# Optimization experiments

Measured on AMD Instinct MI355X. Metric: run time of the kernel, lower is better.

Reference implementation:

```python
import jax, jax.numpy as jnp
import numpy as np

E = 1024
FF = 4096
B, S = 4, 2048
EPS = 1e-5

def _layernorm(x, g, b):
    m = jnp.mean(x, axis=-1, keepdims=True)
    v = jnp.var(x, axis=-1, keepdims=True)
    return (x - m) * jax.lax.rsqrt(v + EPS) * g + b

def setup_inputs() -> dict:
    key = jax.random.key(0)
    ks = jax.random.split(key, 16)
    def lin(k, fan_in, shape):
        bound = 1.0 / np.sqrt(fan_in)
        return jax.random.uniform(k, shape, jnp.float32, -bound, bound)
    return {
        "src_embs": jax.random.normal(ks[0], (B, S, E), jnp.float32),
        "Wq_w": lin(ks[1], E, (E, E)), "Wq_b": lin(ks[2], E, (E,)),
        "Wk_w": lin(ks[3], E, (E, E)), "Wk_b": lin(ks[4], E, (E,)),
        "Wv_w": lin(ks[5], E, (E, E)), "Wv_b": lin(ks[6], E, (E,)),
        "Wo_w": lin(ks[7], E, (E, E)), "Wo_b": lin(ks[8], E, (E,)),
        "W1_w": lin(ks[9], E, (FF, E)), "W1_b": lin(ks[10], E, (FF,)),
        "W2_w": lin(ks[11], FF, (E, FF)), "W2_b": lin(ks[12], FF, (E,)),
        "g1": jnp.ones((E,), jnp.float32), "b1": jnp.zeros((E,), jnp.float32),
        "g2": jnp.ones((E,), jnp.float32), "b2": jnp.zeros((E,), jnp.float32),
        "g3": jnp.ones((E,), jnp.float32), "b3": jnp.zeros((E,), jnp.float32),
    }

def reference(src_embs, Wq_w, Wq_b, Wk_w, Wk_b, Wv_w, Wv_b, Wo_w, Wo_b,
              W1_w, W1_b, W2_w, W2_b, g1, b1, g2, b2, g3, b3):
    x = _layernorm(src_embs, g1, b1)
    Q = x @ Wq_w.T + Wq_b
    K = x @ Wk_w.T + Wk_b
    V = x @ Wv_w.T + Wv_b
    # single-head attention, scaled by sqrt(embed_dim) per source
    scores = jnp.einsum('bqe,bke->bqk', Q, K) / jnp.sqrt(jnp.float32(E))
    attn = jax.nn.softmax(scores, axis=-1)
    attn_out = jnp.einsum('bqk,bke->bqe', attn, V) @ Wo_w.T + Wo_b
    h = src_embs + attn_out
    hn = _layernorm(h, g2, b2)
    ff = jax.nn.relu(hn @ W1_w.T + W1_b) @ W2_w.T + W2_b
    out = h + ff
    return _layernorm(out, g3, b3)
```

## Files before the change

### kernel.cpp

```cpp
#include <hip/hip_runtime.h>
#include <cstdint>
#include <cmath>

#define E_DIM 1024
#define FF_DIM 4096
#define B_DIM 4
#define S_DIM 2048
#define NTOK (B_DIM * S_DIM)
#define QKV_N 3072

typedef __bf16 bf16;
typedef __attribute__((ext_vector_type(8))) __bf16 bf16x8;
typedef __attribute__((ext_vector_type(4))) float f32x4;

__device__ __forceinline__ void gload_lds16(const void* g, void* l) {
  __builtin_amdgcn_global_load_lds(
      (const __attribute__((address_space(1))) unsigned int*)g,
      (__attribute__((address_space(3))) unsigned int*)l, 16, 0, 0);
}

__device__ __forceinline__ float waveRedSum(float v) {
#pragma unroll
  for (int o = 32; o > 0; o >>= 1) v += __shfl_xor(v, o, 64);
  return v;
}
__device__ __forceinline__ float waveRedMax(float v) {
#pragma unroll
  for (int o = 32; o > 0; o >>= 1) v = fmaxf(v, __shfl_xor(v, o, 64));
  return v;
}

__global__ __launch_bounds__(256) void cvt_k(const float* __restrict__ in,
                                             bf16* __restrict__ out, int n4) {
  int i = blockIdx.x * 256 + threadIdx.x;
  if (i < n4) {
    float4 v = reinterpret_cast<const float4*>(in)[i];
    bf16* o = out + (size_t)i * 4;
    o[0] = (bf16)v.x; o[1] = (bf16)v.y; o[2] = (bf16)v.z; o[3] = (bf16)v.w;
  }
}

template <typename OutT>
__global__ __launch_bounds__(256) void layernorm_k(const float* __restrict__ x,
                                                   OutT* __restrict__ out,
                                                   const float* __restrict__ g,
                                                   const float* __restrict__ b) {
  const int row = blockIdx.x;
  const int tid = threadIdx.x;
  const float4 v = reinterpret_cast<const float4*>(x + (size_t)row * E_DIM)[tid];
  float s = v.x + v.y + v.z + v.w;
  float q = v.x * v.x + v.y * v.y + v.z * v.z + v.w * v.w;
  s = waveRedSum(s);
  q = waveRedSum(q);
  __shared__ float sa[4], sb[4];
  const int lane = tid & 63, wid = tid >> 6;
  if (lane == 0) { sa[wid] = s; sb[wid] = q; }
  __syncthreads();
  s = sa[0] + sa[1] + sa[2] + sa[3];
  q = sb[0] + sb[1] + sb[2] + sb[3];
  const float mean = s * (1.0f / E_DIM);
  const float var = q * (1.0f / E_DIM) - mean * mean;
  const float rstd = rsqrtf(var + 1e-5f);
  const int c = tid * 4;
  OutT* op = out + (size_t)row * E_DIM + c;
  const float vv[4] = {v.x, v.y, v.z, v.w};
#pragma unroll
  for (int j = 0; j < 4; ++j)
    op[j] = (OutT)((vv[j] - mean) * rstd * g[c + j] + b[c + j]);
}

__global__ __launch_bounds__(256) void ln3_fused_k(
    const float* __restrict__ h, const bf16* __restrict__ p0,
    const bf16* __restrict__ p1, const float* __restrict__ bias2,
    float* __restrict__ out, const float* __restrict__ g,
    const float* __restrict__ b) {
  const int row = blockIdx.x;
  const int tid = threadIdx.x;
  const int c = tid * 4;
  const float4 hv = reinterpret_cast<const float4*>(h + (size_t)row * E_DIM)[tid];
  const ushort4 a0 = reinterpret_cast<const ushort4*>(p0 + (size_t)row * E_DIM)[tid];
  const ushort4 a1 = reinterpret_cast<const ushort4*>(p1 + (size_t)row * E_DIM)[tid];
  const float4 bv = reinterpret_cast<const float4*>(bias2)[tid];
  auto b2f = [](unsigned short u) {
    union { unsigned int i; float f; } t; t.i = (unsigned int)u << 16; return t.f;
  };
  float x[4];
  x[0] = hv.x + b2f(a0.x) + b2f(a1.x) + bv.x;
  x[1] = hv.y + b2f(a0.y) + b2f(a1.y) + bv.y;
  x[2] = hv.z + b2f(a0.z) + b2f(a1.z) + bv.z;
  x[3] = hv.w + b2f(a0.w) + b2f(a1.w) + bv.w;
  float s = x[0] + x[1] + x[2] + x[3];
  float q = x[0] * x[0] + x[1] * x[1] + x[2] * x[2] + x[3] * x[3];
  s = waveRedSum(s);
  q = waveRedSum(q);
  __shared__ float sa[4], sb[4];
  const int lane = tid & 63, wid = tid >> 6;
  if (lane == 0) { sa[wid] = s; sb[wid] = q; }
  __syncthreads();
  s = sa[0] + sa[1] + sa[2] + sa[3];
  q = sb[0] + sb[1] + sb[2] + sb[3];
  const float mean = s * (1.0f / E_DIM);
  const float var = q * (1.0f / E_DIM) - mean * mean;
  const float rstd = rsqrtf(var + 1e-5f);
  float* op = out + (size_t)row * E_DIM + c;
#pragma unroll
  for (int j = 0; j < 4; ++j)
    op[j] = (x[j] - mean) * rstd * g[c + j] + b[c + j];
}

__global__ __launch_bounds__(256) void softmax_k(bf16* __restrict__ scores) {
  const int row = blockIdx.x;
  bf16* rp = scores + (size_t)row * S_DIM;
  const int tid = threadIdx.x;
  const int lane = tid & 63, wid = tid >> 6;
  bf16x8 v8 = *reinterpret_cast<const bf16x8*>(rp + tid * 8);
  float v[8];
#pragma unroll
  for (int j = 0; j < 8; ++j) v[j] = (float)v8[j];
  float mx = v[0];
#pragma unroll
  for (int j = 1; j < 8; ++j) mx = fmaxf(mx, v[j]);
  mx = waveRedMax(mx);
  __shared__ float sm_[4], ss_[4];
  if (lane == 0) sm_[wid] = mx;
  __syncthreads();
  mx = fmaxf(fmaxf(sm_[0], sm_[1]), fmaxf(sm_[2], sm_[3]));
  float e[8];
  float s = 0.f;
#pragma unroll
  for (int j = 0; j < 8; ++j) { e[j] = __expf(v[j] - mx); s += e[j]; }
  s = waveRedSum(s);
  if (lane == 0) ss_[wid] = s;
  __syncthreads();
  s = ss_[0] + ss_[1] + ss_[2] + ss_[3];
  const float inv = 1.0f / s;
  bf16x8 o;
#pragma unroll
  for (int j = 0; j < 8; ++j) o[j] = (bf16)(e[j] * inv);
  *reinterpret_cast<bf16x8*>(rp + tid * 8) = o;
}

__global__ __launch_bounds__(256) void transpose_k(const bf16* __restrict__ in,
                                                   int ld_in, size_t bstride_in,
                                                   bf16* __restrict__ out) {
  __shared__ bf16 t[32][33];
  const int b = blockIdx.z;
  const bf16* ip = in + (size_t)b * bstride_in;
  bf16* op = out + (size_t)b * S_DIM * E_DIM;
  const int e0 = blockIdx.x * 32, s0 = blockIdx.y * 32;
  const int tx = threadIdx.x & 31, ty = threadIdx.x >> 5;
#pragma unroll
  for (int r = 0; r < 32; r += 8)
    t[ty + r][tx] = ip[(size_t)(s0 + ty + r) * ld_in + e0 + tx];
  __syncthreads();
#pragma unroll
  for (int r = 0; r < 32; r += 8)
    op[(size_t)(e0 + ty + r) * S_DIM + s0 + tx] = t[tx][ty + r];
}

template <int BN, typename OutT, bool RELU>
__global__ __launch_bounds__(512) void gemm8p_k(
    const bf16* __restrict__ A0, int lda, const bf16* __restrict__ Bt0, int ldb,
    OutT* __restrict__ C0, int ldc, int M, int N, int K,
    const float* __restrict__ bias, const float* __restrict__ resid, int ldr,
    float scale, size_t sAz, size_t sBz, size_t sCz) {
  constexpr int BM = 256;
  constexpr int NCH_B = BN / 64;
  constexpr int NCH = 4 + NCH_B;
  constexpr int DEPTH = (BN == 256) ? 2 : 3;
  constexpr int DBUF = (BM + BN) * 128;
  __shared__ __align__(16) char smem[DEPTH * DBUF];

  const int tid = threadIdx.x;
  const int lane = tid & 63;
  const int wid = tid >> 6;

  const bf16* A = A0 + (size_t)blockIdx.z * sAz;
  const bf16* Bt = Bt0 + (size_t)blockIdx.z * sBz;
  OutT* C = C0 + (size_t)blockIdx.z * sCz;

  const int gx = gridDim.x;
  const int nwg = gx * gridDim.y;
  int wg = blockIdx.y * gx + blockIdx.x;
  {
    const int q = nwg >> 3, r8 = nwg & 7;
    const int xcd = wg & 7, lin = wg >> 3;
    wg = (xcd < r8 ? xcd * (q + 1) : r8 * (q + 1) + (xcd - r8) * q) + lin;
  }
  const int m0 = (wg / gx) * 256;
  const int n0 = (wg % gx) * BN;

  auto stage_chunk = [&](int t, int c) {
    char* base = smem + (t % DEPTH) * DBUF;
    const int r8 = tid >> 3;
    const int gg = tid & 7;
    if (c < NCH_B) {
      const int row = c * 64 + r8;
      const int g = gg ^ (row & 7);
      gload_lds16(Bt + (size_t)(n0 + row) * ldb + t * 64 + g * 8,
                  base + BM * 128 + c * 8192 + wid * 1024);
    } else {
      const int i = c - NCH_B;
      const int ca = ((i & 1) << 1) | (i >> 1);
      const int row = ca * 64 + r8;
      const int g = gg ^ (row & 7);
      gload_lds16(A + (size_t)(m0 + row) * lda + t * 64 + g * 8,
                  base + ca * 8192 + wid * 1024);
    }
  };

  f32x4 accQ[2][4][2][2] = {};
  f32x4 accH[4][4] = {};

  const int NT = K >> 6;
  if constexpr (BN == 256) {
#pragma unroll
    for (int c = 0; c < NCH; ++c) stage_chunk(0, c);
    asm volatile("s_waitcnt vmcnt(2)" ::: "memory");
  } else {
#pragma unroll
    for (int c = 0; c < NCH; ++c) stage_chunk(0, c);
#pragma unroll
    for (int c = 0; c < NCH; ++c) stage_chunk(1, c);
    asm volatile("s_waitcnt vmcnt(6)" ::: "memory");
  }
  __builtin_amdgcn_s_barrier();

  for (int t = 0; t < NT; ++t) {
    const char* lA = smem + (t % DEPTH) * DBUF;
    const char* lB = lA + BM * 128;
    if constexpr (BN == 256) {
      const int wr = wid >> 2;
      const int wc = wid & 3;
      bf16x8 af[4][2];
      bf16x8 bfv[2][2][2];
#pragma unroll
      for (int p = 0; p < 4; ++p) {
        const int mh = p >> 1, nh = p & 1;
        if (p == 0 || p == 2) {
#pragma unroll
          for (int fm = 0; fm < 4; ++fm) {
            const int row = wr * 128 + mh * 64 + fm * 16 + (lane & 15);
#pragma unroll
            for (int ks = 0; ks < 2; ++ks) {
              const int g = ((ks << 2) | (lane >> 4)) ^ (row & 7);
              af[fm][ks] = *reinterpret_cast<const bf16x8*>(lA + row * 128 + g * 16);
            }
          }
        }
        if (p < 2) {
#pragma unroll
          for (int fn = 0; fn < 2; ++fn) {
            const int row = wc * 64 + p * 32 + fn * 16 + (lane & 15);
#pragma unroll
            for (int ks = 0; ks < 2; ++ks) {
              const int g = ((ks << 2) | (lane >> 4)) ^ (row & 7);
              bfv[p][fn][ks] =
                  *reinterpret_cast<const bf16x8*>(lB + row * 128 + g * 16);
            }
          }
        }
        if (t + 1 < NT) {
#pragma unroll
          for (int c = 0; c < 2; ++c) stage_chunk(t + 1, p * 2 + c);
        }
        __builtin_amdgcn_s_barrier();
        __builtin_amdgcn_s_setprio(1);
#pragma unroll
        for (int fm = 0; fm < 4; ++fm)
#pragma unroll
          for (int fn = 0; fn < 2; ++fn) {
            accQ[mh][fm][nh][fn] = __builtin_amdgcn_mfma_f32_16x16x32_bf16(
                af[fm][0], bfv[nh][fn][0], accQ[mh][fm][nh][fn], 0, 0, 0);
            accQ[mh][fm][nh][fn] = __builtin_amdgcn_mfma_f32_16x16x32_bf16(
                af[fm][1], bfv[nh][fn][1], accQ[mh][fm][nh][fn], 0, 0, 0);
          }
        __builtin_amdgcn_s_setprio(0);
        if (p == 1) {
          if (t + 1 < NT) asm volatile("s_waitcnt vmcnt(4)" ::: "memory");
          else            asm volatile("s_waitcnt vmcnt(0)" ::: "memory");
        }
        if (p == 3) {
          asm volatile("s_waitcnt vmcnt(2)" ::: "memory");
        }
        __builtin_amdgcn_s_barrier();
      }
    } else {
      const int wr = wid >> 1;
      const int wc = wid & 1;
#pragma unroll
      for (int p = 0; p < 2; ++p) {
        bf16x8 af[4], bf[4];
#pragma unroll
        for (int fm = 0; fm < 4; ++fm) {
          const int row = wr * 64 + fm * 16 + (lane & 15);
          const int g = ((p << 2) | (lane >> 4)) ^ (row & 7);
          af[fm] = *reinterpret_cast<const bf16x8*>(lA + row * 128 + g * 16);
        }
#pragma unroll
        for (int fn = 0; fn < 4; ++fn) {
          const int row = wc * 64 + fn * 16 + (lane & 15);
          const int g = ((p << 2) | (lane >> 4)) ^ (row & 7);
          bf[fn] = *reinterpret_cast<const bf16x8*>(lB + row * 128 + g * 16);
        }
        if (t + 2 < NT) {
#pragma unroll
          for (int c = 0; c < 3; ++c) stage_chunk(t + 2, p * 3 + c);
        }
        __builtin_amdgcn_s_barrier();
        __builtin_amdgcn_s_setprio(1);
#pragma unroll
        for (int fm = 0; fm < 4; ++fm)
#pragma unroll
          for (int fn = 0; fn < 4; ++fn)
            accH[fm][fn] = __builtin_amdgcn_mfma_f32_16x16x32_bf16(
                af[fm], bf[fn], accH[fm][fn], 0, 0, 0);
        __builtin_amdgcn_s_setprio(0);
        if (p == 1) {
          if (t + 2 < NT) asm volatile("s_waitcnt vmcnt(6)" ::: "memory");
          else            asm volatile("s_waitcnt vmcnt(0)" ::: "memory");
        }
        __builtin_amdgcn_s_barrier();
      }
    }
  }

  if constexpr (BN == 256) {
    const int wr = wid >> 2, wc = wid & 3;
#pragma unroll
    for (int mh = 0; mh < 2; ++mh)
#pragma unroll
      for (int nh = 0; nh < 2; ++nh)
#pragma unroll
        for (int fn = 0; fn < 2; ++fn) {
          const int col = n0 + wc * 64 + nh * 32 + fn * 16 + (lane & 15);
          const float bv = bias ? bias[col] : 0.0f;
#pragma unroll
          for (int fm = 0; fm < 4; ++fm)
#pragma unroll
            for (int i = 0; i < 4; ++i) {
              const int row = m0 + wr * 128 + mh * 64 + fm * 16 + (lane >> 4) * 4 + i;
              float v = accQ[mh][fm][nh][fn][i] * scale + bv;
              if (resid) v += resid[(size_t)row * ldr + col];
              if (RELU) v = fmaxf(v, 0.0f);
              C[(size_t)row * ldc + col] = (OutT)v;
            }
        }
  } else {
    const int wr = wid >> 1, wc = wid & 1;
#pragma unroll
    for (int fn = 0; fn < 4; ++fn) {
      const int col = n0 + wc * 64 + fn * 16 + (lane & 15);
      const float bv = bias ? bias[col] : 0.0f;
#pragma unroll
      for (int fm = 0; fm < 4; ++fm)
#pragma unroll
        for (int i = 0; i < 4; ++i) {
          const int row = m0 + wr * 64 + fm * 16 + (lane >> 4) * 4 + i;
          float v = accH[fm][fn][i] * scale + bv;
          if (resid) v += resid[(size_t)row * ldr + col];
          if (RELU) v = fmaxf(v, 0.0f);
          C[(size_t)row * ldc + col] = (OutT)v;
        }
    }
  }
}

extern "C" void kernel_launch(void* const* d_in, const int* in_sizes, int n_in,
                              void* d_out, int out_size, void* d_ws,
                              size_t ws_size, hipStream_t stream) {
  const float* src = (const float*)d_in[0];
  const float* Wq_w = (const float*)d_in[1];
  const float* Wq_b = (const float*)d_in[2];
  const float* Wk_w = (const float*)d_in[3];
  const float* Wk_b = (const float*)d_in[4];
  const float* Wv_w = (const float*)d_in[5];
  const float* Wv_b = (const float*)d_in[6];
  const float* Wo_w = (const float*)d_in[7];
  const float* Wo_b = (const float*)d_in[8];
  const float* W1_w = (const float*)d_in[9];
  const float* W1_b = (const float*)d_in[10];
  const float* W2_w = (const float*)d_in[11];
  const float* W2_b = (const float*)d_in[12];
  const float* g1 = (const float*)d_in[13];
  const float* b1 = (const float*)d_in[14];
  const float* g2 = (const float*)d_in[15];
  const float* b2 = (const float*)d_in[16];
  const float* g3 = (const float*)d_in[17];
  const float* b3 = (const float*)d_in[18];
  float* out = (float*)d_out;
  (void)ws_size; (void)in_sizes; (void)n_in; (void)out_size;

  const size_t MB = 1ull << 20;
  char* ws = (char*)d_ws;
  bf16* wqkv = (bf16*)(ws + 0 * MB);
  bf16* wo = (bf16*)(ws + 6 * MB);
  bf16* w1 = (bf16*)(ws + 8 * MB);
  bf16* w2 = (bf16*)(ws + 16 * MB);
  bf16* Cqkv = (bf16*)(ws + 24 * MB);
  bf16* Vt = (bf16*)(ws + 72 * MB);
  bf16* scoresB = (bf16*)(ws + 88 * MB);
  bf16* xln = (bf16*)(ws + 88 * MB);
  float* bqkv = (float*)(ws + 104 * MB);
  bf16* ctx = Cqkv;
  bf16* hn = scoresB;
  bf16* f1 = (bf16*)(ws + 24 * MB);
  bf16* pp = (bf16*)(ws + 88 * MB);
  float* h = out;

  cvt_k<<<(E_DIM * E_DIM / 4 + 255) / 256, 256, 0, stream>>>(Wq_w, wqkv, E_DIM * E_DIM / 4);
  cvt_k<<<(E_DIM * E_DIM / 4 + 255) / 256, 256, 0, stream>>>(Wk_w, wqkv + (size_t)E_DIM * E_DIM, E_DIM * E_DIM / 4);
  cvt_k<<<(E_DIM * E_DIM / 4 + 255) / 256, 256, 0, stream>>>(Wv_w, wqkv + 2 * (size_t)E_DIM * E_DIM, E_DIM * E_DIM / 4);
  cvt_k<<<(E_DIM * E_DIM / 4 + 255) / 256, 256, 0, stream>>>(Wo_w, wo, E_DIM * E_DIM / 4);
  cvt_k<<<(FF_DIM * E_DIM / 4 + 255) / 256, 256, 0, stream>>>(W1_w, w1, FF_DIM * E_DIM / 4);
  cvt_k<<<(FF_DIM * E_DIM / 4 + 255) / 256, 256, 0, stream>>>(W2_w, w2, FF_DIM * E_DIM / 4);
  hipMemcpyAsync(bqkv, Wq_b, E_DIM * 4, hipMemcpyDeviceToDevice, stream);
  hipMemcpyAsync(bqkv + E_DIM, Wk_b, E_DIM * 4, hipMemcpyDeviceToDevice, stream);
  hipMemcpyAsync(bqkv + 2 * E_DIM, Wv_b, E_DIM * 4, hipMemcpyDeviceToDevice, stream);

  layernorm_k<bf16><<<NTOK, 256, 0, stream>>>(src, xln, g1, b1);

  dim3 gQKV(QKV_N / 256, NTOK / 256);
  gemm8p_k<256, bf16, false><<<gQKV, 512, 0, stream>>>(
      xln, E_DIM, wqkv, E_DIM, Cqkv, QKV_N, NTOK, QKV_N, E_DIM,
      bqkv, nullptr, 0, 1.0f, 0, 0, 0);

  dim3 gSc(S_DIM / 256, S_DIM / 256, B_DIM);
  gemm8p_k<256, bf16, false><<<gSc, 512, 0, stream>>>(
      Cqkv, QKV_N, Cqkv + E_DIM, QKV_N, scoresB, S_DIM, S_DIM, S_DIM, E_DIM,
      nullptr, nullptr, 0, 1.0f / 32.0f,
      (size_t)S_DIM * QKV_N, (size_t)S_DIM * QKV_N, (size_t)S_DIM * S_DIM);

  softmax_k<<<B_DIM * S_DIM, 256, 0, stream>>>(scoresB);

  transpose_k<<<dim3(E_DIM / 32, S_DIM / 32, B_DIM), 256, 0, stream>>>(
      Cqkv + 2 * E_DIM, QKV_N, (size_t)S_DIM * QKV_N, Vt);

  dim3 gPV(E_DIM / 128, S_DIM / 256, B_DIM);
  gemm8p_k<128, bf16, false><<<gPV, 512, 0, stream>>>(
      scoresB, S_DIM, Vt, S_DIM, ctx, E_DIM, S_DIM, E_DIM, S_DIM,
      nullptr, nullptr, 0, 1.0f,
      (size_t)S_DIM * S_DIM, (size_t)S_DIM * E_DIM, (size_t)S_DIM * E_DIM);

  dim3 gWo(E_DIM / 128, NTOK / 256);
  gemm8p_k<128, float, false><<<gWo, 512, 0, stream>>>(
      ctx, E_DIM, wo, E_DIM, h, E_DIM, NTOK, E_DIM, E_DIM,
      Wo_b, src, E_DIM, 1.0f, 0, 0, 0);

  layernorm_k<bf16><<<NTOK, 256, 0, stream>>>(h, hn, g2, b2);

  dim3 gF1(FF_DIM / 256, NTOK / 256);
  gemm8p_k<256, bf16, true><<<gF1, 512, 0, stream>>>(
      hn, E_DIM, w1, E_DIM, f1, FF_DIM, NTOK, FF_DIM, E_DIM,
      W1_b, nullptr, 0, 1.0f, 0, 0, 0);

  dim3 gF2(E_DIM / 256, NTOK / 256, 2);
  gemm8p_k<256, bf16, false><<<gF2, 512, 0, stream>>>(
      f1, FF_DIM, w2, FF_DIM, pp, E_DIM, NTOK, E_DIM, FF_DIM / 2,
      nullptr, nullptr, 0, 1.0f,
      (size_t)(FF_DIM / 2), (size_t)(FF_DIM / 2), (size_t)NTOK * E_DIM);

  ln3_fused_k<<<NTOK, 256, 0, stream>>>(
      h, pp, pp + (size_t)NTOK * E_DIM, W2_b, out, g3, b3);
}
```

Baseline: 399.8 us.

## Stage GEMM tiles through registers instead of direct global-to-LDS loads

Replaces the global_load_lds asynchronous copy pipeline (2-3 deep LDS ring) with register staging: each thread loads the next K-tile into int4 registers at the start of an iteration and writes them to a double-buffered LDS slot at the end. Address computation is hoisted into precomputed pointers and offsets. This cuts LDS use for the BN=128 path and removes the interleaved per-phase vmcnt waits, at the cost of extra VGPRs, explicit LDS stores, and a shallower prefetch that may expose global latency.

```diff
diff --git a/kernel.cpp b/kernel.cpp
--- a/kernel.cpp
+++ b/kernel.cpp
@@ -12,12 +12,6 @@
 typedef __bf16 bf16;
 typedef __attribute__((ext_vector_type(8))) __bf16 bf16x8;
 typedef __attribute__((ext_vector_type(4))) float f32x4;
-
-__device__ __forceinline__ void gload_lds16(const void* g, void* l) {
-  __builtin_amdgcn_global_load_lds(
-      (const __attribute__((address_space(1))) unsigned int*)g,
-      (__attribute__((address_space(3))) unsigned int*)l, 16, 0, 0);
-}
 
 __device__ __forceinline__ float waveRedSum(float v) {
 #pragma unroll
@@ -167,9 +161,8 @@
   constexpr int BM = 256;
   constexpr int NCH_B = BN / 64;
   constexpr int NCH = 4 + NCH_B;
-  constexpr int DEPTH = (BN == 256) ? 2 : 3;
   constexpr int DBUF = (BM + BN) * 128;
-  __shared__ __align__(16) char smem[DEPTH * DBUF];
+  __shared__ __align__(16) char smem[2 * DBUF];
 
   const int tid = threadIdx.x;
   const int lane = tid & 63;
@@ -190,45 +183,47 @@
   const int m0 = (wg / gx) * 256;
   const int n0 = (wg % gx) * BN;
 
-  auto stage_chunk = [&](int t, int c) {
-    char* base = smem + (t % DEPTH) * DBUF;
+  const bf16* gp[NCH];
+  int loff[NCH];
+  {
     const int r8 = tid >> 3;
     const int gg = tid & 7;
-    if (c < NCH_B) {
-      const int row = c * 64 + r8;
-      const int g = gg ^ (row & 7);
-      gload_lds16(Bt + (size_t)(n0 + row) * ldb + t * 64 + g * 8,
-                  base + BM * 128 + c * 8192 + wid * 1024);
-    } else {
-      const int i = c - NCH_B;
-      const int ca = ((i & 1) << 1) | (i >> 1);
-      const int row = ca * 64 + r8;
-      const int g = gg ^ (row & 7);
-      gload_lds16(A + (size_t)(m0 + row) * lda + t * 64 + g * 8,
-                  base + ca * 8192 + wid * 1024);
+#pragma unroll
+    for (int c = 0; c < NCH; ++c) {
+      if (c < NCH_B) {
+        const int row = c * 64 + r8;
+        const int g = gg ^ (row & 7);
+        gp[c] = Bt + (size_t)(n0 + row) * ldb + g * 8;
+        loff[c] = BM * 128 + c * 8192 + tid * 16;
+      } else {
+        const int i = c - NCH_B;
+        const int ca = ((i & 1) << 1) | (i >> 1);
+        const int row = ca * 64 + r8;
+        const int g = gg ^ (row & 7);
+        gp[c] = A + (size_t)(m0 + row) * lda + g * 8;
+        loff[c] = ca * 8192 + tid * 16;
+      }
     }
-  };
+  }
 
   f32x4 accQ[2][4][2][2] = {};
   f32x4 accH[4][4] = {};
+  int4 stg[NCH];
 
   const int NT = K >> 6;
-  if constexpr (BN == 256) {
-#pragma unroll
-    for (int c = 0; c < NCH; ++c) stage_chunk(0, c);
-    asm volatile("s_waitcnt vmcnt(2)" ::: "memory");
-  } else {
-#pragma unroll
-    for (int c = 0; c < NCH; ++c) stage_chunk(0, c);
-#pragma unroll
-    for (int c = 0; c < NCH; ++c) stage_chunk(1, c);
-    asm volatile("s_waitcnt vmcnt(6)" ::: "memory");
-  }
+#pragma unroll
+  for (int c = 0; c < NCH; ++c) stg[c] = *reinterpret_cast<const int4*>(gp[c]);
+#pragma unroll
+  for (int c = 0; c < NCH; ++c)
+    *reinterpret_cast<int4*>(smem + loff[c]) = stg[c];
+  asm volatile("s_waitcnt lgkmcnt(0)" ::: "memory");
   __builtin_amdgcn_s_barrier();
 
   for (int t = 0; t < NT; ++t) {
-    const char* lA = smem + (t % DEPTH) * DBUF;
+    const char* lA = smem + (t & 1) * DBUF;
     const char* lB = lA + BM * 128;
+    char* wbuf = smem + ((t + 1) & 1) * DBUF;
+    const bool pf = (t + 1 < NT);
     if constexpr (BN == 256) {
       const int wr = wid >> 2;
       const int wc = wid & 3;
@@ -237,6 +232,12 @@
 #pragma unroll
       for (int p = 0; p < 4; ++p) {
         const int mh = p >> 1, nh = p & 1;
+        if (p == 0 && pf) {
+#pragma unroll
+          for (int c = 0; c < NCH; ++c)
+            stg[c] = *reinterpret_cast<const int4*>(gp[c] + (t + 1) * 64);
+          __builtin_amdgcn_sched_barrier(0);
+        }
         if (p == 0 || p == 2) {
 #pragma unroll
           for (int fm = 0; fm < 4; ++fm) {
@@ -259,10 +260,6 @@
                   *reinterpret_cast<const bf16x8*>(lB + row * 128 + g * 16);
             }
           }
-        }
-        if (t + 1 < NT) {
-#pragma unroll
-          for (int c = 0; c < 2; ++c) stage_chunk(t + 1, p * 2 + c);
         }
         __builtin_amdgcn_s_barrier();
         __builtin_amdgcn_s_setprio(1);
@@ -276,12 +273,11 @@
                 af[fm][1], bfv[nh][fn][1], accQ[mh][fm][nh][fn], 0, 0, 0);
           }
         __builtin_amdgcn_s_setprio(0);
-        if (p == 1) {
-          if (t + 1 < NT) asm volatile("s_waitcnt vmcnt(4)" ::: "memory");
-          else            asm volatile("s_waitcnt vmcnt(0)" ::: "memory");
-        }
-        if (p == 3) {
-          asm volatile("s_waitcnt vmcnt(2)" ::: "memory");
+        if (p == 3 && pf) {
+#pragma unroll
+          for (int c = 0; c < NCH; ++c)
+            *reinterpret_cast<int4*>(wbuf + loff[c]) = stg[c];
+          asm volatile("s_waitcnt lgkmcnt(0)" ::: "memory");
         }
         __builtin_amdgcn_s_barrier();
       }
@@ -290,6 +286,12 @@
       const int wc = wid & 1;
 #pragma unroll
       for (int p = 0; p < 2; ++p) {
+        if (p == 0 && pf) {
+#pragma unroll
+          for (int c = 0; c < NCH; ++c)
+            stg[c] = *reinterpret_cast<const int4*>(gp[c] + (t + 1) * 64);
+          __builtin_amdgcn_sched_barrier(0);
+        }
         bf16x8 af[4], bf[4];
 #pragma unroll
         for (int fm = 0; fm < 4; ++fm) {
@@ -303,10 +305,6 @@
           const int g = ((p << 2) | (lane >> 4)) ^ (row & 7);
           bf[fn] = *reinterpret_cast<const bf16x8*>(lB + row * 128 + g * 16);
         }
-        if (t + 2 < NT) {
-#pragma unroll
-          for (int c = 0; c < 3; ++c) stage_chunk(t + 2, p * 3 + c);
-        }
         __builtin_amdgcn_s_barrier();
         __builtin_amdgcn_s_setprio(1);
 #pragma unroll
@@ -316,9 +314,11 @@
             accH[fm][fn] = __builtin_amdgcn_mfma_f32_16x16x32_bf16(
                 af[fm], bf[fn], accH[fm][fn], 0, 0, 0);
         __builtin_amdgcn_s_setprio(0);
-        if (p == 1) {
-          if (t + 2 < NT) asm volatile("s_waitcnt vmcnt(6)" ::: "memory");
-          else            asm volatile("s_waitcnt vmcnt(0)" ::: "memory");
+        if (p == 1 && pf) {
+#pragma unroll
+          for (int c = 0; c < NCH; ++c)
+            *reinterpret_cast<int4*>(wbuf + loff[c]) = stg[c];
+          asm volatile("s_waitcnt lgkmcnt(0)" ::: "memory");
         }
         __builtin_amdgcn_s_barrier();
       }
```

New measurement: 854.2 us. +113.7%, slower.
